# Optimization experiments

Measured on AMD Instinct MI355X. Metric: run time of the kernel, lower is better.

The kernel has to match this reference:

```python
import jax, jax.numpy as jnp
import numpy as np

B, T, D, H = 4096, 204800, 32, 64
EPS = 1e-10


def setup_inputs() -> dict:
    key = jax.random.key(0)
    ks = jax.random.split(key, 6)
    candidate = jax.random.normal(ks[0], (B, D), dtype=jnp.float32)
    behavior_values = jax.random.normal(ks[1], (T, D), dtype=jnp.float32)
    row_ids = jnp.sort(jax.random.randint(ks[2], (T,), 0, B, dtype=jnp.int32))
    in_dim = D + D + D * D  # concat of candidate, behavior, flattened outer product
    W1 = jax.random.normal(ks[3], (in_dim, H), dtype=jnp.float32) * (1.0 / np.sqrt(in_dim))
    b1 = jnp.zeros((H,), dtype=jnp.float32)
    alpha = jnp.zeros((H,), dtype=jnp.float32)  # Dice alpha init 0
    W2 = jax.random.normal(ks[4], (H, 1), dtype=jnp.float32) * (1.0 / np.sqrt(H))
    b2 = jnp.zeros((1,), dtype=jnp.float32)
    return {"candidate": candidate, "behavior_values": behavior_values,
            "row_ids": row_ids, "W1": W1, "b1": b1, "alpha": alpha,
            "W2": W2, "b2": b2}


def dice(x, alpha):
    mean = jnp.mean(x, axis=-1, keepdims=True)
    std = jnp.sqrt(jnp.mean(jnp.square(x - mean) + EPS, axis=-1, keepdims=True))
    p = jax.nn.sigmoid((x - mean) / (std + EPS))
    return alpha * (1.0 - p) * x + p * x


def reference(candidate, behavior_values, row_ids, W1, b1, alpha, W2, b2):
    # gather candidate embedding for each behavior row: [T, D]
    cand_per_behavior = candidate[row_ids]
    # outer product: behavior[:, :, None] * candidate[:, None, :] -> [T, D, D]
    outer = behavior_values[:, :, None] * cand_per_behavior[:, None, :]
    outer_flat = outer.reshape(outer.shape[0], D * D)  # [T, D*D]
    feat = jnp.concatenate([cand_per_behavior, behavior_values, outer_flat], axis=1)
    h = feat @ W1 + b1                 # [T, H]
    h = dice(h, alpha)
    w = h @ W2 + b2                    # [T, 1]
    weighted = behavior_values * w     # [T, D]
    out = jax.ops.segment_sum(weighted, row_ids, num_segments=B)  # [B, D]
    return out
```

## Files before the change

kernel.cpp:

```cpp
#include <hip/hip_runtime.h>
#include <cstddef>

#define DICE_EPS 1e-10f

typedef __attribute__((ext_vector_type(8))) short bf16x8;
typedef __attribute__((ext_vector_type(4))) float f32x4;

__device__ inline void f2bf_split(float x, short& hi, short& lo) {
  const unsigned u = __float_as_uint(x);
  hi = (short)(u >> 16);
  const float rem = x - __uint_as_float(u & 0xffff0000u);
  lo = (short)(__float_as_uint(rem) >> 16);
}

#define DPP_ADD(v, ctrl)                                             \
  ((v) + __int_as_float(__builtin_amdgcn_update_dpp(                 \
             0, __float_as_int(v), (ctrl), 0xF, 0xF, true)))
#define REDUCE16(v)            \
  do {                         \
    v = DPP_ADD(v, 0xB1);      \
    v = DPP_ADD(v, 0x4E);      \
    v = DPP_ADD(v, 0x128);     \
    v = DPP_ADD(v, 0x124);     \
  } while (0)

__global__ __launch_bounds__(1024) void attention_fused(
    const float* __restrict__ cand, const float* __restrict__ behavior,
    const int* __restrict__ row_ids, const float* __restrict__ W1,
    const float* __restrict__ b1, const float* __restrict__ alpha,
    const float* __restrict__ W2, const float* __restrict__ b2,
    float* __restrict__ out, int T, int B) {
  const int lane = threadIdx.x & 63;
  const int w = threadIdx.x >> 6;
  const int r0 = blockIdx.x * 16;
  const int r = r0 + w;
  const int c = lane & 15;
  const int g = lane >> 4;

  __shared__ __align__(16) unsigned short img[16 * 2048];

  int t0, t1;
  {
    int lo = 0, hi = T;
    while (lo < hi) { int mid = (lo + hi) >> 1; if (row_ids[mid] < r) lo = mid + 1; else hi = mid; }
    t0 = lo;
    hi = T;
    while (lo < hi) { int mid = (lo + hi) >> 1; if (row_ids[mid] < r + 1) lo = mid + 1; else hi = mid; }
    t1 = lo;
  }

  bf16x8 Ahi, Alo;
  {
    const f32x4* ap =
        reinterpret_cast<const f32x4*>(cand + (size_t)(r0 + c) * 32 + 8 * g);
    const f32x4 a0 = ap[0], a1 = ap[1];
    const float av[8] = {a0.x, a0.y, a0.z, a0.w, a1.x, a1.y, a1.z, a1.w};
#pragma unroll
    for (int j = 0; j < 8; j++) {
      short h, l;
      f2bf_split(av[j], h, l);
      Ahi[j] = h; Alo[j] = l;
    }
  }

  float v[8][4];
#pragma unroll
  for (int m = 0; m < 8; m++) {
    const int np = 8 * w + m;
    const int i = np >> 2;
    const int k = 16 * (np & 3) + c;
    const float* bp = W1 + (size_t)(64 + 32 * i + 8 * g) * 64 + k;
    bf16x8 Bh, Bl;
#pragma unroll
    for (int jj = 0; jj < 8; jj++) {
      short h, l;
      f2bf_split(bp[(size_t)jj * 64], h, l);
      Bh[jj] = h; Bl[jj] = l;
    }
    f32x4 Cz = {0.f, 0.f, 0.f, 0.f};
    Cz = __builtin_amdgcn_mfma_f32_16x16x32_bf16(Alo, Bh, Cz, 0, 0, 0);
    Cz = __builtin_amdgcn_mfma_f32_16x16x32_bf16(Ahi, Bl, Cz, 0, 0, 0);
    Cz = __builtin_amdgcn_mfma_f32_16x16x32_bf16(Ahi, Bh, Cz, 0, 0, 0);
    const float bias = W1[(size_t)(32 + i) * 64 + k];
#pragma unroll
    for (int p = 0; p < 4; p++) v[m][p] = Cz[p] + bias;
  }

  bf16x8 Bhi[4], Blo[4];
#pragma unroll
  for (int m = 0; m < 8; m++) {
    const int np = 8 * w + m;
    const int base = ((np & 3) * 64 + 16 * (np >> 5) + c) * 8 + ((np >> 2) & 7);
#pragma unroll
    for (int p = 0; p < 4; p++) {
      const unsigned u = __float_as_uint(v[m][p]);
      img[(4 * g + p) * 2048 + base] = (unsigned short)(u >> 16);
    }
  }
  __syncthreads();
#pragma unroll
  for (int n = 0; n < 4; n++)
    Bhi[n] = *reinterpret_cast<const bf16x8*>(&img[w * 2048 + (n * 64 + lane) * 8]);
  __syncthreads();
#pragma unroll
  for (int m = 0; m < 8; m++) {
    const int np = 8 * w + m;
    const int base = ((np & 3) * 64 + 16 * (np >> 5) + c) * 8 + ((np >> 2) & 7);
#pragma unroll
    for (int p = 0; p < 4; p++) {
      const float x = v[m][p];
      const float rem = x - __uint_as_float(__float_as_uint(x) & 0xffff0000u);
      img[(4 * g + p) * 2048 + base] = (unsigned short)(__float_as_uint(rem) >> 16);
    }
  }
  __syncthreads();
#pragma unroll
  for (int n = 0; n < 4; n++)
    Blo[n] = *reinterpret_cast<const bf16x8*>(&img[w * 2048 + (n * 64 + lane) * 8]);

  float base_n[4], al_n[4], w2_n[4];
#pragma unroll
  for (int n = 0; n < 4; n++) {
    base_n[n] = b1[16 * n + c];
    al_n[n] = alpha[16 * n + c];
    w2_n[n] = W2[16 * n + c];
  }
  for (int d = 0; d < 32; d++) {
    const float cd = cand[(size_t)r * 32 + d];
#pragma unroll
    for (int n = 0; n < 4; n++)
      base_n[n] = fmaf(cd, W1[(size_t)d * 64 + 16 * n + c], base_n[n]);
  }
  const float b2v = b2[0];
  const int wsrc = ((c >> 2) << 4) | (c & 3);

  float acc[8];
#pragma unroll
  for (int jj = 0; jj < 8; jj++) acc[jj] = 0.f;

  for (int tb = t0; tb < t1; tb += 16) {
    const int trow = tb + c;
    f32x4 a0 = {0.f, 0.f, 0.f, 0.f}, a1 = {0.f, 0.f, 0.f, 0.f};
    if (trow < t1) {
      const f32x4* bp =
          reinterpret_cast<const f32x4*>(behavior + (size_t)trow * 32 + 8 * g);
      a0 = bp[0];
      a1 = bp[1];
    }
    bf16x8 Fhi, Flo;
    {
      const float av[8] = {a0.x, a0.y, a0.z, a0.w, a1.x, a1.y, a1.z, a1.w};
#pragma unroll
      for (int j = 0; j < 8; j++) {
        short h, l;
        f2bf_split(av[j], h, l);
        Fhi[j] = h; Flo[j] = l;
      }
    }

    f32x4 C[4];
#pragma unroll
    for (int n = 0; n < 4; n++) {
      f32x4 cz = {0.f, 0.f, 0.f, 0.f};
      cz = __builtin_amdgcn_mfma_f32_16x16x32_bf16(Flo, Bhi[n], cz, 0, 0, 0);
      cz = __builtin_amdgcn_mfma_f32_16x16x32_bf16(Fhi, Blo[n], cz, 0, 0, 0);
      cz = __builtin_amdgcn_mfma_f32_16x16x32_bf16(Fhi, Bhi[n], cz, 0, 0, 0);
      C[n] = cz;
    }

    float s[4], s2[4];
#pragma unroll
    for (int j = 0; j < 4; j++) {
      float ss = 0.f, qq = 0.f;
#pragma unroll
      for (int n = 0; n < 4; n++) {
        const float h = C[n][j] + base_n[n];
        C[n][j] = h;
        ss += h;
        qq += h * h;
      }
      s[j] = ss;
      s2[j] = qq;
    }
#pragma unroll
    for (int j = 0; j < 4; j++) {
      REDUCE16(s[j]);
      REDUCE16(s2[j]);
    }

    float wp[4];
#pragma unroll
    for (int j = 0; j < 4; j++) {
      const float mean = s[j] * (1.f / 64.f);
      const float var = fmaxf(s2[j] * (1.f / 64.f) - mean * mean, 0.f);
      const float inv = __builtin_amdgcn_rsqf(var + DICE_EPS);
      float ww = 0.f;
#pragma unroll
      for (int n = 0; n < 4; n++) {
        const float h = C[n][j];
        const float e = __expf((mean - h) * inv);
        const float p = __builtin_amdgcn_rcpf(1.f + e);
        const float hd = (al_n[n] + p * (1.f - al_n[n])) * h;
        ww = fmaf(hd, w2_n[n], ww);
      }
      wp[j] = ww;
    }
#pragma unroll
    for (int j = 0; j < 4; j++) REDUCE16(wp[j]);

    const float t01 = (c & 1) ? wp[1] : wp[0];
    const float t23 = (c & 1) ? wp[3] : wp[2];
    const float vsel = (c & 2) ? t23 : t01;
    const float wv = __shfl(vsel, wsrc, 64) + b2v;

    acc[0] = fmaf(a0.x, wv, acc[0]);
    acc[1] = fmaf(a0.y, wv, acc[1]);
    acc[2] = fmaf(a0.z, wv, acc[2]);
    acc[3] = fmaf(a0.w, wv, acc[3]);
    acc[4] = fmaf(a1.x, wv, acc[4]);
    acc[5] = fmaf(a1.y, wv, acc[5]);
    acc[6] = fmaf(a1.z, wv, acc[6]);
    acc[7] = fmaf(a1.w, wv, acc[7]);
  }

#pragma unroll
  for (int jj = 0; jj < 8; jj++) REDUCE16(acc[jj]);
  if (c == 0) {
    f32x4 o0 = {acc[0], acc[1], acc[2], acc[3]};
    f32x4 o1 = {acc[4], acc[5], acc[6], acc[7]};
    f32x4* op = reinterpret_cast<f32x4*>(out + (size_t)r * 32 + 8 * g);
    op[0] = o0;
    op[1] = o1;
  }
}

extern "C" void kernel_launch(void* const* d_in, const int* in_sizes, int n_in,
                              void* d_out, int out_size, void* d_ws, size_t ws_size,
                              hipStream_t stream) {
  const float* cand     = (const float*)d_in[0];
  const float* behavior = (const float*)d_in[1];
  const int*   row_ids  = (const int*)d_in[2];
  const float* W1       = (const float*)d_in[3];
  const float* b1       = (const float*)d_in[4];
  const float* alpha    = (const float*)d_in[5];
  const float* W2       = (const float*)d_in[6];
  const float* b2       = (const float*)d_in[7];
  float* out = (float*)d_out;

  const int B = in_sizes[0] / 32;
  const int T = in_sizes[2];

  attention_fused<<<B / 16, 1024, 0, stream>>>(cand, behavior, row_ids, W1, b1,
                                               alpha, W2, b2, out, T, B);
}
```

Baseline: 109.0 us.

## Use wave-cooperative segment search, share bounds via LDS, and prefetch behavior rows

Replaces each wave's two serial binary searches over row_ids with a 64-way ballot search. Segment starts are shared through shared memory, so only one extra search runs per block for the end bound. The first behavior tile is loaded early so its latency overlaps the W1 setup, and the main loop prefetches the next tile while computing the current one. This cuts dependent global-load latency in the prologue and loop, at the cost of extra registers and a ballot-based search that issues more memory reads per step.

New measurement: 102.1 us. -6.4%, faster.

```diff
diff --git a/kernel.cpp b/kernel.cpp
--- a/kernel.cpp
+++ b/kernel.cpp
@@ -23,6 +23,23 @@
     v = DPP_ADD(v, 0x128);     \
     v = DPP_ADD(v, 0x124);     \
   } while (0)
+
+__device__ inline int lower_bound_coop(const int* __restrict__ arr, int n,
+                                       int target, int lane) {
+  int lo = 0, hi = n;
+  while (hi > lo) {
+    const int stride = (hi - lo + 63) >> 6;
+    const int pos = lo + lane * stride;
+    const int v = (pos < hi) ? arr[pos] : 0x7fffffff;
+    const unsigned long long m = __ballot(v < target);
+    const int cnt = __popcll(m);
+    if (cnt == 0) break;
+    const int nlo = lo + (cnt - 1) * stride + 1;
+    hi = min(lo + cnt * stride, hi);
+    lo = nlo;
+  }
+  return lo;
+}
 
 __global__ __launch_bounds__(1024) void attention_fused(
     const float* __restrict__ cand, const float* __restrict__ behavior,
@@ -38,23 +55,32 @@
   const int g = lane >> 4;
 
   __shared__ __align__(16) unsigned short img[16 * 2048];
-
-  int t0, t1;
+  __shared__ int segs[17];
+
+  const int t0 = lower_bound_coop(row_ids, T, r, lane);
+  if (lane == 0) segs[w] = t0;
+  if (w == 15) {
+    const int te = lower_bound_coop(row_ids, T, r0 + 16, lane);
+    if (lane == 0) segs[16] = te;
+  }
+
+  f32x4 a0 = {0.f, 0.f, 0.f, 0.f}, a1 = {0.f, 0.f, 0.f, 0.f};
   {
-    int lo = 0, hi = T;
-    while (lo < hi) { int mid = (lo + hi) >> 1; if (row_ids[mid] < r) lo = mid + 1; else hi = mid; }
-    t0 = lo;
-    hi = T;
-    while (lo < hi) { int mid = (lo + hi) >> 1; if (row_ids[mid] < r + 1) lo = mid + 1; else hi = mid; }
-    t1 = lo;
+    const int trow = t0 + c;
+    if (trow < T) {
+      const f32x4* bp =
+          reinterpret_cast<const f32x4*>(behavior + (size_t)trow * 32 + 8 * g);
+      a0 = bp[0];
+      a1 = bp[1];
+    }
   }
 
   bf16x8 Ahi, Alo;
   {
     const f32x4* ap =
         reinterpret_cast<const f32x4*>(cand + (size_t)(r0 + c) * 32 + 8 * g);
-    const f32x4 a0 = ap[0], a1 = ap[1];
-    const float av[8] = {a0.x, a0.y, a0.z, a0.w, a1.x, a1.y, a1.z, a1.w};
+    const f32x4 x0 = ap[0], x1 = ap[1];
+    const float av[8] = {x0.x, x0.y, x0.z, x0.w, x1.x, x1.y, x1.z, x1.w};
 #pragma unroll
     for (int j = 0; j < 8; j++) {
       short h, l;
@@ -134,19 +160,28 @@
   const float b2v = b2[0];
   const int wsrc = ((c >> 2) << 4) | (c & 3);
 
+  const int t1 = segs[w + 1];
+  if (t0 + c >= t1) {
+    a0 = (f32x4){0.f, 0.f, 0.f, 0.f};
+    a1 = (f32x4){0.f, 0.f, 0.f, 0.f};
+  }
+
   float acc[8];
 #pragma unroll
   for (int jj = 0; jj < 8; jj++) acc[jj] = 0.f;
 
   for (int tb = t0; tb < t1; tb += 16) {
-    const int trow = tb + c;
-    f32x4 a0 = {0.f, 0.f, 0.f, 0.f}, a1 = {0.f, 0.f, 0.f, 0.f};
-    if (trow < t1) {
-      const f32x4* bp =
-          reinterpret_cast<const f32x4*>(behavior + (size_t)trow * 32 + 8 * g);
-      a0 = bp[0];
-      a1 = bp[1];
-    }
+    f32x4 n0 = {0.f, 0.f, 0.f, 0.f}, n1 = {0.f, 0.f, 0.f, 0.f};
+    {
+      const int trow = tb + 16 + c;
+      if (trow < t1) {
+        const f32x4* bp =
+            reinterpret_cast<const f32x4*>(behavior + (size_t)trow * 32 + 8 * g);
+        n0 = bp[0];
+        n1 = bp[1];
+      }
+    }
+
     bf16x8 Fhi, Flo;
     {
       const float av[8] = {a0.x, a0.y, a0.z, a0.w, a1.x, a1.y, a1.z, a1.w};
@@ -221,6 +256,9 @@
     acc[5] = fmaf(a1.y, wv, acc[5]);
     acc[6] = fmaf(a1.z, wv, acc[6]);
     acc[7] = fmaf(a1.w, wv, acc[7]);
+
+    a0 = n0;
+    a1 = n1;
   }
 
 #pragma unroll
```
